# Kernel tuning notes

Measured on AMD Instinct MI355X. Metric: run time of the kernel, lower is better.

## Reference

```python
import jax, jax.numpy as jnp
import numpy as np

jax.config.update("jax_enable_x64", True)  # int64 keys for lattice hashing

_EPS = float(np.finfo(np.float64).eps)
_SIGMA_SPATIAL = 5.0   # spatial stddev (voxels)
_SIGMA_COLOR = 0.25    # intensity stddev
_BASE = 8192           # per-coordinate key range
_OFF = 4096            # coordinate offset so packed keys are non-negative


def _encode(coords):
    """Pack (..., d) integer lattice coords into a single int64 key."""
    enc = jnp.zeros(coords.shape[:-1], jnp.int64)
    for i in range(coords.shape[-1]):
        enc = enc * _BASE + (coords[..., i].astype(jnp.int64) + _OFF)
    return enc


def _bilateral_features(image):
    """Bilateral features: (z,y,x)/sigma_s and intensity/sigma_c. image: (1,D,H,W)."""
    _, D, H, W = image.shape
    z, y, x = jnp.meshgrid(jnp.arange(D, dtype=jnp.float32),
                           jnp.arange(H, dtype=jnp.float32),
                           jnp.arange(W, dtype=jnp.float32), indexing="ij")
    spatial = jnp.stack([z, y, x], -1) / _SIGMA_SPATIAL            # (D,H,W,3)
    color = (image[0] / _SIGMA_COLOR)[..., None]                   # (D,H,W,1)
    return jnp.concatenate([spatial, color], -1).reshape(-1, 4)    # (N,4)


def _permutohedral(q, feats):
    """Permutohedral-lattice Gaussian filtering (splat -> blur -> slice).
    q: (N,C) float32 values, feats: (N,d) float32 positions. Returns (N,C).
    Global scale of the blur kernel cancels in the final normalization."""
    N, d = feats.shape
    dp1 = d + 1
    # ---- elevate features onto the hyperplane H_d ----
    inv_std = np.sqrt(2.0 / 3.0) * dp1
    scale = jnp.asarray([inv_std / np.sqrt((i + 1) * (i + 2)) for i in range(d)], jnp.float32)
    cf = feats * scale
    elev = [None] * dp1
    sm = jnp.zeros((N,), jnp.float32)
    for i in range(d, 0, -1):
        c = cf[:, i - 1]
        elev[i] = sm - i * c
        sm = sm + c
    elev[0] = sm
    elevated = jnp.stack(elev, axis=1)                             # (N, d+1)
    # ---- closest remainder-0 lattice point ----
    rd = jnp.round(elevated / dp1)
    rem0 = rd * dp1
    sum_rd = jnp.sum(rd, axis=1).astype(jnp.int32)
    # ---- rank of each coordinate (ties broken by index) ----
    diff = elevated - rem0
    di = diff[:, :, None]
    dj = diff[:, None, :]
    jlt = (jnp.arange(dp1)[None, :] < jnp.arange(dp1)[:, None])[None]  # mask[i,j] = j < i
    rank = jnp.sum((dj > di) | ((dj == di) & jlt), axis=2).astype(jnp.int32)
    rank = rank + sum_rd[:, None]
    low, high = rank < 0, rank > d
    rank = rank + jnp.where(low, dp1, 0) - jnp.where(high, dp1, 0)
    rem0 = rem0 + jnp.where(low, float(dp1), 0.0) - jnp.where(high, float(dp1), 0.0)
    # ---- barycentric coordinates inside the enclosing simplex ----
    v = (elevated - rem0) / dp1
    rows = jnp.arange(N)[:, None]
    bary = jnp.zeros((N, d + 2), jnp.float32)
    bary = bary.at[rows, d - rank].add(v)
    bary = bary.at[rows, dp1 - rank].add(-v)
    bary = bary.at[:, 0].add(1.0 + bary[:, dp1])
    bary = bary[:, :dp1]                                           # (N, d+1) weights per remainder
    # ---- integer keys of the d+1 simplex vertices (first d coords suffice) ----
    rem0i = rem0[:, :d].astype(jnp.int32)
    keys = jnp.stack([rem0i + jnp.where(rank[:, :d] < dp1 - r, r, r - dp1).astype(jnp.int32)
                      for r in range(dp1)], axis=1)                # (N, d+1, d)
    enc = _encode(keys).reshape(-1)
    Mpad = N * dp1
    sentinel = _BASE ** d                                          # > any real key; sorts last
    uniq, inv = jnp.unique(enc, return_inverse=True, size=Mpad, fill_value=sentinel)
    inv = inv.reshape(N, dp1)
    # ---- splat ----
    C = q.shape[1]
    vals = jnp.zeros((Mpad, C), jnp.float32).at[inv].add(bary[:, :, None] * q[:, None, :])
    # ---- blur along each of the d+1 lattice directions ----
    coords = jnp.stack([(uniq // (_BASE ** (d - 1 - i))) % _BASE - _OFF for i in range(d)],
                       axis=-1).astype(jnp.int32)                  # (Mpad, d)

    def lookup(c):
        e = _encode(c)
        pos = jnp.clip(jnp.searchsorted(uniq, e), 0, Mpad - 1)
        return pos, uniq[pos] == e

    for j in range(dp1):
        off = jnp.ones((d,), jnp.int32)
        if j < d:
            off = off.at[j].set(-d)
        p1, f1 = lookup(coords + off)
        p2, f2 = lookup(coords - off)
        n1 = jnp.where(f1[:, None], vals[p1], 0.0)
        n2 = jnp.where(f2[:, None], vals[p2], 0.0)
        vals = 0.5 * vals + 0.25 * (n1 + n2)
    # ---- slice ----
    return jnp.sum(bary[:, :, None] * vals[inv], axis=1)           # (N, C)


def setup_inputs():
    key = jax.random.key(0)
    k1, k2 = jax.random.split(key)
    input_ = jax.random.uniform(k1, (4, 96, 96, 96), dtype=jnp.float32)
    image = jax.random.uniform(k2, (1, 96, 96, 96), dtype=jnp.float32)
    return {"input_": input_, "image": image}


def reference(input_, image):
    feats = _bilateral_features(image)
    C, D, H, W = input_.shape
    q = input_.reshape(C, -1).T                                    # (N, C)
    ones = jnp.ones((q.shape[0], 1), jnp.float32)                  # fused normalization pass
    filt = _permutohedral(jnp.concatenate([q, ones], axis=1), feats)
    out = filt[:, :C] / (filt[:, C:] + _EPS)                       # == permuto(q) * 1/(permuto(1)+eps)
    return out.T.reshape(C, D, H, W)
```

## Files before the change

kernel.cpp:

```cpp
#include <hip/hip_runtime.h>
#include <hip/hip_fp16.h>
#include <stdint.h>

#define NPTS (96*96*96)
#define NP5  (NPTS*5)

#define GD1 33
#define GD2 29
#define GD3 25
#define GO0 5
#define GO1 16
#define GO2 18
#define GO3 19
#define GS3 5
#define GS2 (GD3*GS3)
#define GS1 (GD2*GS2)
#define GS0 (GD1*GS1)
#define GCELLS (31*GS0)
#define GCELLS1 (GCELLS+1)
#define GSSUM (GS0+GS1+GS2+GS3)

#define LHS 2048

struct LatPt { int cell[5]; float w[5]; };
struct V5 { float s0, s1, s2, s3, w; };


#define LATTICE_MATH(n)                                                        \
  int x = n % 96, y = (n / 96) % 96, z = n / (96 * 96);                        \
  float cf[4];                                                                 \
  cf[0] = ((float)z / 5.0f) * 2.8867513459481287f;                             \
  cf[1] = ((float)y / 5.0f) * 1.6666666666666667f;                             \
  cf[2] = ((float)x / 5.0f) * 1.1785113019775793f;                             \
  cf[3] = (imgv / 0.25f) * 0.9128709291752769f;                                \
  float elev[5];                                                               \
  float sm = 0.f;                                                              \
  _Pragma("unroll")                                                            \
  for (int i = 4; i >= 1; --i){ float c = cf[i-1]; elev[i] = sm - (float)i * c; sm += c; } \
  elev[0] = sm;                                                                \
  float rem0[5]; float sumrd_f = 0.f;                                          \
  _Pragma("unroll")                                                            \
  for (int i = 0; i < 5; i++){ float rd = rintf(elev[i] / 5.0f); rem0[i] = rd * 5.0f; sumrd_f += rd; } \
  int sum_rd = (int)sumrd_f;                                                   \
  float diff[5];                                                               \
  _Pragma("unroll")                                                            \
  for (int i = 0; i < 5; i++) diff[i] = elev[i] - rem0[i];                     \
  int rank[5];                                                                 \
  _Pragma("unroll")                                                            \
  for (int i = 0; i < 5; i++){                                                 \
    int r = 0;                                                                 \
    _Pragma("unroll")                                                          \
    for (int j = 0; j < 5; j++){                                               \
      r += (diff[j] > diff[i] || (diff[j] == diff[i] && j < i)) ? 1 : 0;       \
    }                                                                          \
    rank[i] = r + sum_rd;                                                      \
  }                                                                            \
  _Pragma("unroll")                                                            \
  for (int i = 0; i < 5; i++){                                                 \
    if (rank[i] < 0)      { rank[i] += 5; rem0[i] += 5.0f; }                   \
    else if (rank[i] > 4) { rank[i] -= 5; rem0[i] -= 5.0f; }                   \
  }                                                                            \
  float b[6] = {0.f,0.f,0.f,0.f,0.f,0.f};                                      \
  _Pragma("unroll")                                                            \
  for (int i = 0; i < 5; i++){                                                 \
    float v = (elev[i] - rem0[i]) / 5.0f;                                      \
    b[4 - rank[i]] += v;                                                       \
    b[5 - rank[i]] -= v;                                                       \
  }                                                                            \
  b[0] += 1.0f + b[5];                                                         \
  int rem0i[4];                                                                \
  _Pragma("unroll")                                                            \
  for (int i = 0; i < 4; i++) rem0i[i] = (int)rem0[i];

__device__ __forceinline__ LatPt lat_compute(int n, float imgv)
{
  LATTICE_MATH(n)
  LatPt p;
  #pragma unroll
  for (int r = 0; r < 5; r++){
    int q0 = (rem0i[0] / 5) - (rank[0] < 5 - r ? 0 : 1) + GO0;
    int q1 = (rem0i[1] / 5) - (rank[1] < 5 - r ? 0 : 1) + GO1;
    int q2 = (rem0i[2] / 5) - (rank[2] < 5 - r ? 0 : 1) + GO2;
    int q3 = (rem0i[3] / 5) - (rank[3] < 5 - r ? 0 : 1) + GO3;
    int cell = (((q0 * GD1 + q1) * GD2 + q2) * GD3 + q3) * 5 + r;
    if ((unsigned)cell >= (unsigned)GCELLS) cell = GCELLS;
    p.cell[r] = cell;
    p.w[r] = b[r];
  }
  return p;
}

__global__ void k_build_hyb(const float* __restrict__ image,
                            const float* __restrict__ input_,
                            int* __restrict__ head,
                            int4* __restrict__ nodes)
{
  __shared__ int   ls_cell[LHS];
  __shared__ int   ls_head[LHS];
  __shared__ short ls_next[1280];
  __shared__ float ls_w[1280];
  __shared__ float ls_q[256 * 4];
  __shared__ short ls_slot[1280];
  __shared__ int   ls_cnt;

  int tid = threadIdx.x;
  #pragma unroll
  for (int i = 0; i < LHS / 256; i++){
    ls_cell[tid + 256 * i] = -1;
    ls_head[tid + 256 * i] = -1;
  }
  if (tid == 0) ls_cnt = 0;
  __syncthreads();

  int n = blockIdx.x * 256 + tid;
  float q0 = input_[n], q1 = input_[NPTS + n], q2 = input_[2 * NPTS + n], q3 = input_[3 * NPTS + n];
  *reinterpret_cast<float4*>(&ls_q[tid * 4]) = make_float4(q0, q1, q2, q3);
  LatPt P = lat_compute(n, image[n]);

  #pragma unroll
  for (int r = 0; r < 5; r++){
    int cell = P.cell[r];
    unsigned int h = ((unsigned int)cell * 2654435761u) & (LHS - 1);
    while (true){
      int prev = atomicCAS(&ls_cell[h], -1, cell);
      if (prev == -1){
        int li = atomicAdd(&ls_cnt, 1);
        ls_slot[li] = (short)h;
        break;
      }
      if (prev == cell) break;
      h = (h + 1) & (LHS - 1);
    }
    int e = tid * 5 + r;
    ls_w[e] = P.w[r];
    ls_next[e] = (short)atomicExch(&ls_head[h], e);
  }
  __syncthreads();

  int cnt = ls_cnt;
  int blockBase = blockIdx.x * 1280;
  for (int i = tid; i < cnt; i += 256){
    int slot = ls_slot[i];
    int cell = ls_cell[slot];
    float s0 = 0.f, s1 = 0.f, s2 = 0.f, s3 = 0.f, s4 = 0.f;
    int e = ls_head[slot];
    while (e >= 0){
      int en = ls_next[e];
      float w = ls_w[e];
      float4 q = *reinterpret_cast<const float4*>(&ls_q[(e / 5) * 4]);
      s0 += w * q.x; s1 += w * q.y; s2 += w * q.z; s3 += w * q.w; s4 += w;
      e = en;
    }
    int node = blockBase + i;
    int old = atomicExch(&head[cell], node);
    __half2 h01 = __floats2half2_rn(s0, s1);
    __half2 h23 = __floats2half2_rn(s2, s3);
    int4 raw;
    raw.x = old;
    raw.y = *reinterpret_cast<int*>(&h01);
    raw.z = *reinterpret_cast<int*>(&h23);
    raw.w = __float_as_int(s4);
    nodes[node] = raw;
  }
}

__global__ void k_gather_agg(const int* __restrict__ head,
                             const int4* __restrict__ nodes,
                             int3* __restrict__ vals,
                             unsigned int* __restrict__ bitmap)
{
  int c = blockIdx.x * blockDim.x + threadIdx.x;
  int e = -1;
  if (c < GCELLS1) e = head[c];
  bool occ = (e >= 0);
  unsigned long long mask = __ballot(occ);
  int lane = threadIdx.x & 63;
  if (lane == 0)       bitmap[c >> 5] = (unsigned int)(mask & 0xffffffffu);
  else if (lane == 32) bitmap[c >> 5] = (unsigned int)(mask >> 32);
  if (c >= GCELLS1) return;

  float s0 = 0.f, s1 = 0.f, s2 = 0.f, s3 = 0.f, s4 = 0.f;
  while (e >= 0){
    int4 raw = nodes[e];
    __half2 h01 = *reinterpret_cast<__half2*>(&raw.y);
    __half2 h23 = *reinterpret_cast<__half2*>(&raw.z);
    float2 f01 = __half22float2(h01);
    float2 f23 = __half22float2(h23);
    s0 += f01.x; s1 += f01.y; s2 += f23.x; s3 += f23.y;
    s4 += __int_as_float(raw.w);
    e = raw.x;
  }
  __half2 o01 = __floats2half2_rn(s0, s1);
  __half2 o23 = __floats2half2_rn(s2, s3);
  int3 rec;
  rec.x = *reinterpret_cast<int*>(&o01);
  rec.y = *reinterpret_cast<int*>(&o23);
  rec.z = __float_as_int(s4);
  vals[c] = rec;
}

__device__ __forceinline__ V5 ublur(const unsigned int* __restrict__ bitmap,
                                    const int3* __restrict__ vin,
                                    int d, int dPa, int dPb, int dMa, int dMb)
{
  V5 u = {0.f, 0.f, 0.f, 0.f, 0.f};
  unsigned int wd = bitmap[d >> 5];
  if (!((wd >> (d & 31)) & 1u)) return u;
  int rd = d % 5;
  int p1 = d + (rd == 4 ? dPb : dPa);
  int p2 = d + (rd == 0 ? dMb : dMa);
  int3 a  = vin[d];
  int3 b1 = vin[p1];
  int3 b2 = vin[p2];
  float2 a01 = __half22float2(*reinterpret_cast<__half2*>(&a.x));
  float2 a23 = __half22float2(*reinterpret_cast<__half2*>(&a.y));
  float2 m01 = __half22float2(*reinterpret_cast<__half2*>(&b1.x));
  float2 m23 = __half22float2(*reinterpret_cast<__half2*>(&b1.y));
  float2 n01 = __half22float2(*reinterpret_cast<__half2*>(&b2.x));
  float2 n23 = __half22float2(*reinterpret_cast<__half2*>(&b2.y));
  u.s0 = 0.5f * a01.x + 0.25f * (m01.x + n01.x);
  u.s1 = 0.5f * a01.y + 0.25f * (m01.y + n01.y);
  u.s2 = 0.5f * a23.x + 0.25f * (m23.x + n23.x);
  u.s3 = 0.5f * a23.y + 0.25f * (m23.y + n23.y);
  u.w  = 0.5f * __int_as_float(a.z) + 0.25f * (__int_as_float(b1.z) + __int_as_float(b2.z));
  return u;
}

__global__ void k_blur2_d(const unsigned int* __restrict__ bitmap,
                          const int3* __restrict__ vin,
                          int3* __restrict__ vout,
                          int dPaA, int dPbA, int dMaA, int dMbA,
                          int dPaB, int dPbB, int dMaB, int dMbB, int zfill)
{
  int c = blockIdx.x * blockDim.x + threadIdx.x;
  if (c >= GCELLS) return;
  unsigned int w = bitmap[c >> 5];
  if (!((w >> (c & 31)) & 1u)){
    if (zfill){
      int3 zero; zero.x = 0; zero.y = 0; zero.z = 0;
      vout[c] = zero;
    }
    return;
  }
  int r = c % 5;
  int q1 = c + (r == 4 ? dPbB : dPaB);
  int q2 = c + (r == 0 ? dMbB : dMaB);

  V5 uc = ublur(bitmap, vin, c,  dPaA, dPbA, dMaA, dMbA);
  V5 u1 = ublur(bitmap, vin, q1, dPaA, dPbA, dMaA, dMbA);
  V5 u2 = ublur(bitmap, vin, q2, dPaA, dPbA, dMaA, dMbA);

  float o0 = 0.5f * uc.s0 + 0.25f * (u1.s0 + u2.s0);
  float o1 = 0.5f * uc.s1 + 0.25f * (u1.s1 + u2.s1);
  float o2 = 0.5f * uc.s2 + 0.25f * (u1.s2 + u2.s2);
  float o3 = 0.5f * uc.s3 + 0.25f * (u1.s3 + u2.s3);
  float ow = 0.5f * uc.w  + 0.25f * (u1.w  + u2.w);

  __half2 o01 = __floats2half2_rn(o0, o1);
  __half2 o23 = __floats2half2_rn(o2, o3);
  int3 rec;
  rec.x = *reinterpret_cast<int*>(&o01);
  rec.y = *reinterpret_cast<int*>(&o23);
  rec.z = __float_as_int(ow);
  vout[c] = rec;
}

__global__ void k_blur_d(const unsigned int* __restrict__ bitmap,
                         const int3* __restrict__ vin,
                         int3* __restrict__ vout,
                         int dPa, int dPb, int dMa, int dMb, int zfill)
{
  int c = blockIdx.x * blockDim.x + threadIdx.x;
  if (c >= GCELLS) return;
  unsigned int w = bitmap[c >> 5];
  if (!((w >> (c & 31)) & 1u)){
    if (zfill){
      int3 zero; zero.x = 0; zero.y = 0; zero.z = 0;
      vout[c] = zero;
    }
    return;
  }
  V5 u = ublur(bitmap, vin, c, dPa, dPb, dMa, dMb);
  __half2 o01 = __floats2half2_rn(u.s0, u.s1);
  __half2 o23 = __floats2half2_rn(u.s2, u.s3);
  int3 rec;
  rec.x = *reinterpret_cast<int*>(&o01);
  rec.y = *reinterpret_cast<int*>(&o23);
  rec.z = __float_as_int(u.w);
  vout[c] = rec;
}

__global__ void k_slice_d(const float* __restrict__ image,
                          const int3* __restrict__ vals,
                          float* __restrict__ out)
{
  int n = blockIdx.x * blockDim.x + threadIdx.x;
  if (n >= NPTS) return;
  LatPt P = lat_compute(n, image[n]);

  float s0 = 0.f, s1 = 0.f, s2 = 0.f, s3 = 0.f, s4 = 0.f;
  #pragma unroll
  for (int r = 0; r < 5; r++){
    float w = P.w[r];
    int3 rec = vals[P.cell[r]];
    float2 f01 = __half22float2(*reinterpret_cast<__half2*>(&rec.x));
    float2 f23 = __half22float2(*reinterpret_cast<__half2*>(&rec.y));
    s0 += w * f01.x; s1 += w * f01.y; s2 += w * f23.x; s3 += w * f23.y;
    s4 += w * __int_as_float(rec.z);
  }
  float denom = s4 + 2.2204460492503131e-16f;
  out[n]            = s0 / denom;
  out[NPTS + n]     = s1 / denom;
  out[2 * NPTS + n] = s2 / denom;
  out[3 * NPTS + n] = s3 / denom;
}


extern "C" void kernel_launch(void* const* d_in, const int* in_sizes, int n_in,
                              void* d_out, int out_size, void* d_ws, size_t ws_size,
                              hipStream_t stream)
{
  const float* input_ = (const float*)d_in[0];
  const float* image  = (const float*)d_in[1];
  float* out = (float*)d_out;
  char* ws = (char*)d_ws;

  const int NB = (NPTS + 255) / 256;
  const int CB = (GCELLS1 + 255) / 256;
  const size_t BMWORDS = (size_t)CB * 8;
  const int Sj[5] = { GS0, GS1, GS2, GS3, 0 };
  int dPa[5], dPb[5], dMa[5], dMb[5];
  for (int j = 0; j < 5; j++){
    dPa[j] = 1 - Sj[j];
    dPb[j] = GSSUM - Sj[j] - 4;
    dMa[j] = Sj[j] - 1;
    dMb[j] = Sj[j] - GSSUM + 4;
  }

  size_t o = 0;
  size_t off_bm   = o; o += BMWORDS * 4;              o = (o + 255) & ~(size_t)255;
  size_t off_dead = o;
  size_t off_head = o; o += (size_t)GCELLS1 * 4;      o = (o + 255) & ~(size_t)255;
  size_t off_node = o; o += (size_t)NP5 * 16;         o = (o + 255) & ~(size_t)255;
  size_t dead_end = o;
  size_t off_vA   = o; o += (size_t)GCELLS1 * 12;
  size_t vB_need  = (size_t)GCELLS1 * 12;
  size_t off_vB   = off_dead;
  if (dead_end - off_dead < vB_need || o > ws_size){
    off_vB = (o + 255) & ~(size_t)255;
  }

  unsigned int* bitmap = (unsigned int*)(ws + off_bm);
  int*          head   = (int*)(ws + off_head);
  int4*         nodes  = (int4*)(ws + off_node);
  int3*         valsA  = (int3*)(ws + off_vA);
  int3*         valsB  = (int3*)(ws + off_vB);

  hipMemsetAsync(head, 0xFF, (size_t)GCELLS1 * 4, stream);

  k_build_hyb<<<NB, 256, 0, stream>>>(image, input_, head, nodes);
  k_gather_agg<<<CB, 256, 0, stream>>>(head, nodes, valsA, bitmap);

  k_blur2_d<<<CB, 256, 0, stream>>>(bitmap, valsA, valsB,
                                    dPa[0], dPb[0], dMa[0], dMb[0],
                                    dPa[1], dPb[1], dMa[1], dMb[1], 1);
  k_blur2_d<<<CB, 256, 0, stream>>>(bitmap, valsB, valsA,
                                    dPa[2], dPb[2], dMa[2], dMb[2],
                                    dPa[3], dPb[3], dMa[3], dMb[3], 0);
  k_blur_d<<<CB, 256, 0, stream>>>(bitmap, valsA, valsB,
                                   dPa[4], dPb[4], dMa[4], dMb[4], 0);

  k_slice_d<<<NB, 256, 0, stream>>>(image, valsB, out);
}
```

Before: 175.3 us.

## Fuse final blur pass into slice kernel and skip unoccupied cells in gather

The last blur direction is no longer a separate full-grid kernel. The slice kernel now computes the blurred value on the fly for each of the 5 lattice cells it touches, which removes one launch and one full read/write pass over the value grid. Gather now returns early for unoccupied cells and relies on a new memset to zero valsA instead of writing zeros. The cost is redundant blur work per point: 5 ublur calls per voxel, each with neighbour lookups, and overlapping cells get recomputed across voxels.

New measurement: 179.9 us. 2.6% more time.

```diff
diff --git a/kernel.cpp b/kernel.cpp
--- a/kernel.cpp
+++ b/kernel.cpp
@@ -177,7 +177,7 @@
   int lane = threadIdx.x & 63;
   if (lane == 0)       bitmap[c >> 5] = (unsigned int)(mask & 0xffffffffu);
   else if (lane == 32) bitmap[c >> 5] = (unsigned int)(mask >> 32);
-  if (c >= GCELLS1) return;
+  if (!occ) return;
 
   float s0 = 0.f, s1 = 0.f, s2 = 0.f, s3 = 0.f, s4 = 0.f;
   while (e >= 0){
@@ -265,34 +265,11 @@
   vout[c] = rec;
 }
 
-__global__ void k_blur_d(const unsigned int* __restrict__ bitmap,
-                         const int3* __restrict__ vin,
-                         int3* __restrict__ vout,
-                         int dPa, int dPb, int dMa, int dMb, int zfill)
-{
-  int c = blockIdx.x * blockDim.x + threadIdx.x;
-  if (c >= GCELLS) return;
-  unsigned int w = bitmap[c >> 5];
-  if (!((w >> (c & 31)) & 1u)){
-    if (zfill){
-      int3 zero; zero.x = 0; zero.y = 0; zero.z = 0;
-      vout[c] = zero;
-    }
-    return;
-  }
-  V5 u = ublur(bitmap, vin, c, dPa, dPb, dMa, dMb);
-  __half2 o01 = __floats2half2_rn(u.s0, u.s1);
-  __half2 o23 = __floats2half2_rn(u.s2, u.s3);
-  int3 rec;
-  rec.x = *reinterpret_cast<int*>(&o01);
-  rec.y = *reinterpret_cast<int*>(&o23);
-  rec.z = __float_as_int(u.w);
-  vout[c] = rec;
-}
-
-__global__ void k_slice_d(const float* __restrict__ image,
+__global__ void k_slice_f(const float* __restrict__ image,
+                          const unsigned int* __restrict__ bitmap,
                           const int3* __restrict__ vals,
-                          float* __restrict__ out)
+                          float* __restrict__ out,
+                          int dPa, int dPb, int dMa, int dMb)
 {
   int n = blockIdx.x * blockDim.x + threadIdx.x;
   if (n >= NPTS) return;
@@ -302,11 +279,9 @@
   #pragma unroll
   for (int r = 0; r < 5; r++){
     float w = P.w[r];
-    int3 rec = vals[P.cell[r]];
-    float2 f01 = __half22float2(*reinterpret_cast<__half2*>(&rec.x));
-    float2 f23 = __half22float2(*reinterpret_cast<__half2*>(&rec.y));
-    s0 += w * f01.x; s1 += w * f01.y; s2 += w * f23.x; s3 += w * f23.y;
-    s4 += w * __int_as_float(rec.z);
+    V5 u = ublur(bitmap, vals, P.cell[r], dPa, dPb, dMa, dMb);
+    s0 += w * u.s0; s1 += w * u.s1; s2 += w * u.s2; s3 += w * u.s3;
+    s4 += w * u.w;
   }
   float denom = s4 + 2.2204460492503131e-16f;
   out[n]            = s0 / denom;
@@ -357,6 +332,7 @@
   int3*         valsB  = (int3*)(ws + off_vB);
 
   hipMemsetAsync(head, 0xFF, (size_t)GCELLS1 * 4, stream);
+  hipMemsetAsync(valsA, 0, (size_t)GCELLS1 * 12, stream);
 
   k_build_hyb<<<NB, 256, 0, stream>>>(image, input_, head, nodes);
   k_gather_agg<<<CB, 256, 0, stream>>>(head, nodes, valsA, bitmap);
@@ -367,8 +343,6 @@
   k_blur2_d<<<CB, 256, 0, stream>>>(bitmap, valsB, valsA,
                                     dPa[2], dPb[2], dMa[2], dMb[2],
                                     dPa[3], dPb[3], dMa[3], dMb[3], 0);
-  k_blur_d<<<CB, 256, 0, stream>>>(bitmap, valsA, valsB,
-                                   dPa[4], dPb[4], dMa[4], dMb[4], 0);
-
-  k_slice_d<<<NB, 256, 0, stream>>>(image, valsB, out);
-}
+  k_slice_f<<<NB, 256, 0, stream>>>(image, bitmap, valsA, out,
+                                    dPa[4], dPb[4], dMa[4], dMb[4]);
+}
```
